# Kernel tuning notes

Hardware: AMD Instinct MI355X
Metric: run time of the kernel (lower is better)

## Reference

```python
import jax, jax.numpy as jnp
import numpy as np

N_NODES = 50000
N_EDGES = 800000
N_FEAT = 512
N_HEADS = 8
OUT_PER_HEAD = 32  # nhid // nheads = 256 // 8
ALPHA = 0.2  # LeakyReLU negative slope


def setup_inputs() -> dict:
    key = jax.random.key(0)
    ks = jax.random.split(key, 7)
    h = jax.random.normal(ks[0], (N_NODES, N_FEAT), dtype=jnp.float32)
    src = jax.random.randint(ks[1], (N_EDGES,), 0, N_NODES)
    dst = jax.random.randint(ks[2], (N_EDGES,), 0, N_NODES)
    # per-head linear W: [H, F, O], bias [H, O]; attention vector a: [H, 2O], bias [H]
    W = jax.random.normal(ks[3], (N_HEADS, N_FEAT, OUT_PER_HEAD), dtype=jnp.float32) * 0.05
    Wb = jax.random.normal(ks[4], (N_HEADS, OUT_PER_HEAD), dtype=jnp.float32) * 0.05
    a = jax.random.normal(ks[5], (N_HEADS, 2 * OUT_PER_HEAD), dtype=jnp.float32) * 0.05
    ab = jax.random.normal(ks[6], (N_HEADS,), dtype=jnp.float32) * 0.05
    return {"h": h, "src": src, "dst": dst, "W": W, "Wb": Wb, "a": a, "ab": ab}


def reference(h, src, dst, W, Wb, a, ab):
    N = h.shape[0]
    H, F_in, O = W.shape
    # Per-head projection Wh = W(h): [N, H, O]
    Wh = jnp.einsum('nf,hfo->nho', h, W) + Wb
    # a @ concat(Wh_src, Wh_dst) == a_src @ Wh_src + a_dst @ Wh_dst
    a_src, a_dst = a[:, :O], a[:, O:]
    e_s = jnp.einsum('nho,ho->nh', Wh, a_src)  # [N, H]
    e_d = jnp.einsum('nho,ho->nh', Wh, a_dst)
    e = e_s[src] + e_d[dst] + ab               # [E, H]
    e = jnp.where(e > 0, e, ALPHA * e)         # LeakyReLU
    # Segment softmax over incoming edges of each destination node
    m = jax.ops.segment_max(e, dst, num_segments=N)        # [N, H]
    m = jnp.where(jnp.isfinite(m), m, jnp.zeros_like(m))   # isolated nodes
    w = jnp.exp(e - m[dst])                                # [E, H]
    denom = jax.ops.segment_sum(w, dst, num_segments=N)    # [N, H]
    att = w / jnp.where(denom[dst] > 0, denom[dst], 1.0)   # [E, H]
    # Weighted aggregation of source projections, per head, then concat heads
    out = jax.ops.segment_sum(att[:, :, None] * Wh[src], dst, num_segments=N)  # [N, H, O]
    return out.reshape(N, H * O)
```

## Files before the change

kernel.cpp:

```cpp
#include <hip/hip_runtime.h>
#include <math.h>

#define ALPHA 0.2f
#define CAP 64

constexpr int F_IN  = 512;
constexpr int HO    = 256;
constexpr int NHEAD = 8;

using bf16x8 = __attribute__((ext_vector_type(8))) short;
using bf16x4 = __attribute__((ext_vector_type(4))) short;
using f32x4  = __attribute__((ext_vector_type(4))) float;

__device__ __forceinline__ ushort f2bf(float f) {
    uint u = __float_as_uint(f);
    uint r = (u + 0x7FFFu + ((u >> 16) & 1u)) >> 16;
    return (ushort)r;
}
__device__ __forceinline__ float bf2f(ushort b) {
    return __uint_as_float(((uint)b) << 16);
}

__global__ __launch_bounds__(256) void prep_kernel(const float* __restrict__ W,
                                                   ushort* __restrict__ Wf,
                                                   const int* __restrict__ dst,
                                                   int* __restrict__ cnt,
                                                   int* __restrict__ rnk, int E) {
    const int bid = blockIdx.x;
    const int t = threadIdx.x;
    if (bid < 64) {
        int g = bid * 256 + t;
        int l   = g & 63;
        int oct = (g >> 6) & 15;
        int ks  = g >> 10;
        int oc  = oct * 16 + (l & 15);
        int hh  = oc >> 5, oo = oc & 31;
        int kb  = ks * 32 + (l >> 4) * 8;
        ushort v[8];
#pragma unroll
        for (int j = 0; j < 8; ++j)
            v[j] = f2bf(W[((size_t)hh * F_IN + kb + j) * 32 + oo]);
        bf16x8 o = { (short)v[0], (short)v[1], (short)v[2], (short)v[3],
                     (short)v[4], (short)v[5], (short)v[6], (short)v[7] };
        *(bf16x8*)(Wf + (size_t)g * 8) = o;
    } else {
        int base = (bid - 64) * 1024;
#pragma unroll
        for (int q = 0; q < 4; ++q) {
            int i = base + q * 256 + t;
            if (i < E) rnk[i] = atomicAdd(&cnt[dst[i]], 1);
        }
    }
}

__global__ __launch_bounds__(256) void scan1_kernel(const int* __restrict__ cnt,
                                                    int* __restrict__ bsum, int N) {
    __shared__ int red[256];
    const int t = threadIdx.x;
    const int b0 = blockIdx.x * 1024;
    int s = 0;
#pragma unroll
    for (int q = 0; q < 4; ++q) {
        int i = b0 + t * 4 + q;
        if (i < N) s += cnt[i];
    }
    red[t] = s;
    __syncthreads();
    for (int st = 128; st > 0; st >>= 1) {
        if (t < st) red[t] += red[t + st];
        __syncthreads();
    }
    if (t == 0) bsum[blockIdx.x] = red[0];
}

__global__ __launch_bounds__(64) void scan2_kernel(int* __restrict__ bsum, int nblk) {
    int l = threadIdx.x;
    int x = (l < nblk) ? bsum[l] : 0;
    int inc = x;
    for (int d = 1; d < 64; d <<= 1) {
        int v = __shfl_up(inc, d);
        if (l >= d) inc += v;
    }
    if (l < nblk) bsum[l] = inc - x;
}

__global__ __launch_bounds__(256) void scan3_kernel(const int* __restrict__ cnt,
                                                    const int* __restrict__ bsum,
                                                    int* __restrict__ off, int N, int E) {
    __shared__ int part[256];
    const int t = threadIdx.x;
    const int b0 = blockIdx.x * 1024;
    int v[4];
    int s = 0;
#pragma unroll
    for (int q = 0; q < 4; ++q) {
        int i = b0 + t * 4 + q;
        v[q] = (i < N) ? cnt[i] : 0;
        s += v[q];
    }
    part[t] = s;
    __syncthreads();
    for (int d = 1; d < 256; d <<= 1) {
        int x = (t >= d) ? part[t - d] : 0;
        __syncthreads();
        part[t] += x;
        __syncthreads();
    }
    int run = bsum[blockIdx.x] + ((t == 0) ? 0 : part[t - 1]);
#pragma unroll
    for (int q = 0; q < 4; ++q) {
        int i = b0 + t * 4 + q;
        if (i < N) { off[i] = run; run += v[q]; }
    }
    if (blockIdx.x == 0 && t == 0) off[N] = E;
}

__global__ __launch_bounds__(256) void place_kernel(const int* __restrict__ src,
                                                    const int* __restrict__ dst,
                                                    const int* __restrict__ rnk,
                                                    const int* __restrict__ off,
                                                    int* __restrict__ se, int E) {
    int base = blockIdx.x * 1024;
#pragma unroll
    for (int q = 0; q < 4; ++q) {
        int i = base + q * 256 + threadIdx.x;
        if (i < E) se[off[dst[i]] + rnk[i]] = src[i];
    }
}

__global__ __launch_bounds__(256, 2) void gemm_kernel(
    const float* __restrict__ h, const ushort* __restrict__ Wf,
    const float* __restrict__ Wb, const float* __restrict__ a,
    ushort* __restrict__ Wh, float* __restrict__ es, float* __restrict__ ed, int N)
{
    __shared__ ushort hs[2][128 * 40];
    const int t = threadIdx.x;
    const int l = t & 63;
    const int w = t >> 6;
    const int l15 = l & 15, l4 = l >> 4;
    const int n0 = blockIdx.x * 128;

    const int sr = t >> 1;
    const int sc = (t & 1) * 16;
    int srow = n0 + sr; if (srow >= N) srow = N - 1;
    const float* hrow = h + (size_t)srow * F_IN + sc;

    f32x4 acc[4][8];
#pragma unroll
    for (int i = 0; i < 4; ++i)
#pragma unroll
        for (int nt = 0; nt < 8; ++nt) acc[i][nt] = (f32x4){0.f, 0.f, 0.f, 0.f};

    {
        float4 v0 = *(const float4*)(hrow);
        float4 v1 = *(const float4*)(hrow + 4);
        float4 v2 = *(const float4*)(hrow + 8);
        float4 v3 = *(const float4*)(hrow + 12);
        bf16x8 o0 = { (short)f2bf(v0.x), (short)f2bf(v0.y), (short)f2bf(v0.z), (short)f2bf(v0.w),
                      (short)f2bf(v1.x), (short)f2bf(v1.y), (short)f2bf(v1.z), (short)f2bf(v1.w) };
        bf16x8 o1 = { (short)f2bf(v2.x), (short)f2bf(v2.y), (short)f2bf(v2.z), (short)f2bf(v2.w),
                      (short)f2bf(v3.x), (short)f2bf(v3.y), (short)f2bf(v3.z), (short)f2bf(v3.w) };
        *(bf16x8*)&hs[0][sr * 40 + sc]     = o0;
        *(bf16x8*)&hs[0][sr * 40 + sc + 8] = o1;
    }
    __syncthreads();

    for (int ks = 0; ks < 16; ++ks) {
        const int cb = ks & 1;
        float4 nx0, nx1, nx2, nx3;
        if (ks < 15) {
            const float* p = hrow + (ks + 1) * 32;
            nx0 = *(const float4*)(p);
            nx1 = *(const float4*)(p + 4);
            nx2 = *(const float4*)(p + 8);
            nx3 = *(const float4*)(p + 12);
        }
        bf16x8 af[4];
#pragma unroll
        for (int i = 0; i < 4; ++i)
            af[i] = *(const bf16x8*)(Wf + ((size_t)((ks * 16 + 4 * w + i) * 64 + l)) * 8);
#pragma unroll
        for (int half = 0; half < 2; ++half) {
            bf16x8 b4[4];
#pragma unroll
            for (int j = 0; j < 4; ++j)
                b4[j] = *(const bf16x8*)&hs[cb][((half * 4 + j) * 16 + l15) * 40 + l4 * 8];
#pragma unroll
            for (int i = 0; i < 4; ++i)
#pragma unroll
                for (int j = 0; j < 4; ++j)
                    acc[i][half * 4 + j] = __builtin_amdgcn_mfma_f32_16x16x32_bf16(
                        af[i], b4[j], acc[i][half * 4 + j], 0, 0, 0);
        }
        if (ks < 15) {
            bf16x8 o0 = { (short)f2bf(nx0.x), (short)f2bf(nx0.y), (short)f2bf(nx0.z), (short)f2bf(nx0.w),
                          (short)f2bf(nx1.x), (short)f2bf(nx1.y), (short)f2bf(nx1.z), (short)f2bf(nx1.w) };
            bf16x8 o1 = { (short)f2bf(nx2.x), (short)f2bf(nx2.y), (short)f2bf(nx2.z), (short)f2bf(nx2.w),
                          (short)f2bf(nx3.x), (short)f2bf(nx3.y), (short)f2bf(nx3.z), (short)f2bf(nx3.w) };
            *(bf16x8*)&hs[cb ^ 1][sr * 40 + sc]     = o0;
            *(bf16x8*)&hs[cb ^ 1][sr * 40 + sc + 8] = o1;
            __syncthreads();
        }
    }

    float4 wb4[4], as4[4], ad4[4];
    int ocb[4];
#pragma unroll
    for (int i = 0; i < 4; ++i) {
        int oc_base = (4 * w + i) * 16 + (l4 << 2);
        ocb[i] = oc_base;
        int head = oc_base >> 5;
        wb4[i] = *(const float4*)(Wb + oc_base);
        as4[i] = *(const float4*)(a + head * 64 + (oc_base & 31));
        ad4[i] = *(const float4*)(a + head * 64 + 32 + (oc_base & 31));
    }
#pragma unroll
    for (int nt = 0; nt < 8; ++nt) {
        int node = n0 + nt * 16 + l15;
        bool ok = node < N;
        float pe[4] = {0.f, 0.f, 0.f, 0.f};
#pragma unroll
        for (int i = 0; i < 4; ++i) {
            f32x4 v = acc[i][nt];
            float r0 = v.x + wb4[i].x, r1 = v.y + wb4[i].y;
            float r2 = v.z + wb4[i].z, r3 = v.w + wb4[i].w;
            if (ok) {
                bf16x4 o = { (short)f2bf(r0), (short)f2bf(r1), (short)f2bf(r2), (short)f2bf(r3) };
                *(bf16x4*)(Wh + (size_t)node * HO + ocb[i]) = o;
            }
            float dsv = r0 * as4[i].x + r1 * as4[i].y + r2 * as4[i].z + r3 * as4[i].w;
            float ddv = r0 * ad4[i].x + r1 * ad4[i].y + r2 * ad4[i].z + r3 * ad4[i].w;
            int hp = i >> 1;
            pe[hp] += dsv; pe[2 + hp] += ddv;
        }
#pragma unroll
        for (int q = 0; q < 4; ++q) {
            pe[q] += __shfl_xor(pe[q], 16);
            pe[q] += __shfl_xor(pe[q], 32);
        }
        if (l4 == 0 && ok) {
            es[(size_t)node * NHEAD + 2 * w]     = pe[0];
            es[(size_t)node * NHEAD + 2 * w + 1] = pe[1];
            ed[(size_t)node * NHEAD + 2 * w]     = pe[2];
            ed[(size_t)node * NHEAD + 2 * w + 1] = pe[3];
        }
    }
}

__global__ __launch_bounds__(256) void node_kernel(
    const int* __restrict__ se, const int* __restrict__ off,
    const float* __restrict__ es, const float* __restrict__ ed,
    const float* __restrict__ ab, const ushort* __restrict__ Wh,
    float* __restrict__ out, int N)
{
    __shared__ float wbuf[4][CAP][NHEAD];
    __shared__ int   sbuf[4][CAP];
    __shared__ float dinv[4][NHEAD];

    const int t = threadIdx.x;
    const int l = t & 63;
    const int wv = t >> 6;
    const int n = blockIdx.x * 4 + wv;
    const bool active = n < N;

    int beg = 0, deg = 0;
    if (active) { beg = off[n]; deg = off[n + 1] - beg; }

    const int slot = l >> 3, hh = l & 7;
    float edn = 0.f, abh = 0.f;
    if (active && deg > 0) {
        edn = ed[(size_t)n * NHEAD + hh];
        abh = ab[hh];
    }

    float dloc = 0.f;
    for (int j = slot; j < deg; j += 8) {
        int s = se[beg + j];
        float ev = es[(size_t)s * NHEAD + hh] + edn + abh;
        ev = ev > 0.f ? ev : ALPHA * ev;
        float wj = __expf(ev);
        if (j < CAP) {
            wbuf[wv][j][hh] = wj;
            if (hh == 0) sbuf[wv][j] = s;
        }
        dloc += wj;
    }
    dloc += __shfl_xor(dloc, 8);
    dloc += __shfl_xor(dloc, 16);
    dloc += __shfl_xor(dloc, 32);
    if (slot == 0) dinv[wv][hh] = (dloc > 0.f) ? 1.f / dloc : 1.f;
    __syncthreads();

    const int oc0 = (l & 31) * 8;
    const int hb  = oc0 >> 5;
    const int par = l >> 5;
    float acc[8] = {0.f, 0.f, 0.f, 0.f, 0.f, 0.f, 0.f, 0.f};

    if (active) {
        const int dcap = deg < CAP ? deg : CAP;
        for (int j = par; j < dcap; j += 2) {
            int s = sbuf[wv][j];
            float wj = wbuf[wv][j][hb];
            bf16x8 row = *(const bf16x8*)(Wh + (size_t)s * HO + oc0);
#pragma unroll
            for (int i = 0; i < 8; ++i)
                acc[i] += wj * bf2f((ushort)row[i]);
        }
        if (deg > CAP) {
            float edb = ed[(size_t)n * NHEAD + hb] + ab[hb];
            for (int j = CAP + par; j < deg; j += 2) {
                int s = se[beg + j];
                float ev = es[(size_t)s * NHEAD + hb] + edb;
                ev = ev > 0.f ? ev : ALPHA * ev;
                float wj = __expf(ev);
                bf16x8 row = *(const bf16x8*)(Wh + (size_t)s * HO + oc0);
#pragma unroll
                for (int i = 0; i < 8; ++i)
                    acc[i] += wj * bf2f((ushort)row[i]);
            }
        }
    }
#pragma unroll
    for (int i = 0; i < 8; ++i) acc[i] += __shfl_xor(acc[i], 32);

    if (active && par == 0) {
        float inv = dinv[wv][hb];
        float4 o0 = make_float4(acc[0] * inv, acc[1] * inv, acc[2] * inv, acc[3] * inv);
        float4 o1 = make_float4(acc[4] * inv, acc[5] * inv, acc[6] * inv, acc[7] * inv);
        *(float4*)(out + (size_t)n * HO + oc0)     = o0;
        *(float4*)(out + (size_t)n * HO + oc0 + 4) = o1;
    }
}

extern "C" void kernel_launch(void* const* d_in, const int* in_sizes, int n_in,
                              void* d_out, int out_size, void* d_ws, size_t ws_size,
                              hipStream_t stream) {
    const float* h   = (const float*)d_in[0];
    const int*   src = (const int*)  d_in[1];
    const int*   dst = (const int*)  d_in[2];
    const float* W   = (const float*)d_in[3];
    const float* Wb  = (const float*)d_in[4];
    const float* a   = (const float*)d_in[5];
    const float* ab  = (const float*)d_in[6];
    float* out = (float*)d_out;

    const int N = in_sizes[0] / F_IN;
    const int E = in_sizes[1];

    auto align_up = [](size_t x) { return (x + 255) & ~size_t(255); };
    char* p = (char*)d_ws;
    ushort* Wh = (ushort*)p; p += align_up((size_t)N * HO * 2);
    float*  es = (float*)p;  p += align_up((size_t)N * NHEAD * 4);
    float*  ed = (float*)p;  p += align_up((size_t)N * NHEAD * 4);
    int* cnt   = (int*)p;    p += align_up((size_t)N * 4);
    int* off   = (int*)p;    p += align_up((size_t)(N + 1) * 4);
    int* rnk   = (int*)p;    p += align_up((size_t)E * 4);
    int* se    = (int*)p;    p += align_up((size_t)E * 4);
    int* bsum  = (int*)p;    p += align_up((size_t)64 * 4);
    ushort* Wf = (ushort*)p; p += align_up((size_t)16 * 16 * 64 * 8 * 2);

    const int nblk = (N + 1023) / 1024;
    const int EB   = (E + 1023) / 1024;
    const int GB   = (N + 127) / 128;

    hipMemsetAsync(cnt, 0, (size_t)N * sizeof(int), stream);
    prep_kernel<<<64 + EB, 256, 0, stream>>>(W, Wf, dst, cnt, rnk, E);
    scan1_kernel<<<nblk, 256, 0, stream>>>(cnt, bsum, N);
    scan2_kernel<<<1, 64, 0, stream>>>(bsum, nblk);
    scan3_kernel<<<nblk, 256, 0, stream>>>(cnt, bsum, off, N, E);
    place_kernel<<<EB, 256, 0, stream>>>(src, dst, rnk, off, se, E);
    gemm_kernel<<<GB, 256, 0, stream>>>(h, Wf, Wb, a, Wh, es, ed, N);
    node_kernel<<<(N + 3) / 4, 256, 0, stream>>>(se, off, es, ed, ab, Wh, out, N);
}
```

Before: 166.8 us.

## Store Wh and scores head-major and split aggregation by head per block

The GEMM now writes Wh as [head][node][32] and es/ed as [head][node] instead of node-major. The aggregation kernel is restructured: each block handles one head for 8 nodes, with one wave per pair of nodes. Softmax weights, the denominator and the weighted sum are computed in a single pass with shuffle reductions, replacing the shared-memory weight buffer, the CAP fallback path and the block barrier. The idea is that blocks sharing a head touch only a 1/8-sized slice of Wh, which should improve cache locality for the gathers. The cost is that se, off and the out row are read and written by eight different blocks, and each gather is only 8 bytes.

Measured after the change: 223.1 us. 1.34x slower.

```diff
diff --git a/kernel.cpp b/kernel.cpp
--- a/kernel.cpp
+++ b/kernel.cpp
@@ -2,7 +2,6 @@
 #include <math.h>
 
 #define ALPHA 0.2f
-#define CAP 64
 
 constexpr int F_IN  = 512;
 constexpr int HO    = 256;
@@ -225,8 +224,9 @@
             float r0 = v.x + wb4[i].x, r1 = v.y + wb4[i].y;
             float r2 = v.z + wb4[i].z, r3 = v.w + wb4[i].w;
             if (ok) {
+                int head = ocb[i] >> 5, oo = ocb[i] & 31;
                 bf16x4 o = { (short)f2bf(r0), (short)f2bf(r1), (short)f2bf(r2), (short)f2bf(r3) };
-                *(bf16x4*)(Wh + (size_t)node * HO + ocb[i]) = o;
+                *(bf16x4*)(Wh + ((size_t)head * N + node) * 32 + oo) = o;
             }
             float dsv = r0 * as4[i].x + r1 * as4[i].y + r2 * as4[i].z + r3 * as4[i].w;
             float ddv = r0 * ad4[i].x + r1 * ad4[i].y + r2 * ad4[i].z + r3 * ad4[i].w;
@@ -239,10 +239,10 @@
             pe[q] += __shfl_xor(pe[q], 32);
         }
         if (l4 == 0 && ok) {
-            es[(size_t)node * NHEAD + 2 * w]     = pe[0];
-            es[(size_t)node * NHEAD + 2 * w + 1] = pe[1];
-            ed[(size_t)node * NHEAD + 2 * w]     = pe[2];
-            ed[(size_t)node * NHEAD + 2 * w + 1] = pe[3];
+            es[(size_t)(2 * w)     * N + node] = pe[0];
+            es[(size_t)(2 * w + 1) * N + node] = pe[1];
+            ed[(size_t)(2 * w)     * N + node] = pe[2];
+            ed[(size_t)(2 * w + 1) * N + node] = pe[3];
         }
     }
 }
@@ -253,82 +253,54 @@
     const float* __restrict__ ab, const ushort* __restrict__ Wh,
     float* __restrict__ out, int N)
 {
-    __shared__ float wbuf[4][CAP][NHEAD];
-    __shared__ int   sbuf[4][CAP];
-    __shared__ float dinv[4][NHEAD];
-
-    const int t = threadIdx.x;
-    const int l = t & 63;
-    const int wv = t >> 6;
-    const int n = blockIdx.x * 4 + wv;
-    const bool active = n < N;
-
-    int beg = 0, deg = 0;
-    if (active) { beg = off[n]; deg = off[n + 1] - beg; }
-
-    const int slot = l >> 3, hh = l & 7;
-    float edn = 0.f, abh = 0.f;
-    if (active && deg > 0) {
-        edn = ed[(size_t)n * NHEAD + hh];
-        abh = ab[hh];
-    }
-
-    float dloc = 0.f;
-    for (int j = slot; j < deg; j += 8) {
-        int s = se[beg + j];
-        float ev = es[(size_t)s * NHEAD + hh] + edn + abh;
-        ev = ev > 0.f ? ev : ALPHA * ev;
-        float wj = __expf(ev);
-        if (j < CAP) {
-            wbuf[wv][j][hh] = wj;
-            if (hh == 0) sbuf[wv][j] = s;
-        }
-        dloc += wj;
-    }
-    dloc += __shfl_xor(dloc, 8);
-    dloc += __shfl_xor(dloc, 16);
-    dloc += __shfl_xor(dloc, 32);
-    if (slot == 0) dinv[wv][hh] = (dloc > 0.f) ? 1.f / dloc : 1.f;
-    __syncthreads();
-
-    const int oc0 = (l & 31) * 8;
-    const int hb  = oc0 >> 5;
-    const int par = l >> 5;
-    float acc[8] = {0.f, 0.f, 0.f, 0.f, 0.f, 0.f, 0.f, 0.f};
-
-    if (active) {
-        const int dcap = deg < CAP ? deg : CAP;
-        for (int j = par; j < dcap; j += 2) {
-            int s = sbuf[wv][j];
-            float wj = wbuf[wv][j][hb];
-            bf16x8 row = *(const bf16x8*)(Wh + (size_t)s * HO + oc0);
-#pragma unroll
-            for (int i = 0; i < 8; ++i)
-                acc[i] += wj * bf2f((ushort)row[i]);
-        }
-        if (deg > CAP) {
-            float edb = ed[(size_t)n * NHEAD + hb] + ab[hb];
-            for (int j = CAP + par; j < deg; j += 2) {
-                int s = se[beg + j];
-                float ev = es[(size_t)s * NHEAD + hb] + edb;
-                ev = ev > 0.f ? ev : ALPHA * ev;
-                float wj = __expf(ev);
-                bf16x8 row = *(const bf16x8*)(Wh + (size_t)s * HO + oc0);
-#pragma unroll
-                for (int i = 0; i < 8; ++i)
-                    acc[i] += wj * bf2f((ushort)row[i]);
-            }
-        }
-    }
-#pragma unroll
-    for (int i = 0; i < 8; ++i) acc[i] += __shfl_xor(acc[i], 32);
-
-    if (active && par == 0) {
-        float inv = dinv[wv][hb];
-        float4 o0 = make_float4(acc[0] * inv, acc[1] * inv, acc[2] * inv, acc[3] * inv);
-        float4 o1 = make_float4(acc[4] * inv, acc[5] * inv, acc[6] * inv, acc[7] * inv);
-        *(float4*)(out + (size_t)n * HO + oc0)     = o0;
-        *(float4*)(out + (size_t)n * HO + oc0 + 4) = o1;
+    const int bid  = blockIdx.x;
+    const int hg   = bid & 7;
+    const int tile = bid >> 3;
+    const int t    = threadIdx.x;
+    const int l    = t & 63;
+    const int wv   = t >> 6;
+    const int slot = l >> 3;
+    const int sub  = l & 7;
+
+    const float abh = ab[hg];
+    const ushort* WhH = Wh + (size_t)hg * N * 32;
+    const float*  esH = es + (size_t)hg * N;
+    const float*  edH = ed + (size_t)hg * N;
+
+#pragma unroll
+    for (int nn = 0; nn < 2; ++nn) {
+        const int n = tile * 8 + wv * 2 + nn;
+        if (n >= N) break;
+        const int beg = off[n];
+        const int deg = off[n + 1] - beg;
+        const float base = edH[n] + abh;
+
+        float a0 = 0.f, a1 = 0.f, a2 = 0.f, a3 = 0.f, dsum = 0.f;
+        for (int j = slot; j < deg; j += 8) {
+            int s = se[beg + j];
+            float ev = esH[s] + base;
+            ev = ev > 0.f ? ev : ALPHA * ev;
+            float wj = __expf(ev);
+            bf16x4 row = *(const bf16x4*)(WhH + (size_t)s * 32 + sub * 4);
+            a0 += wj * bf2f((ushort)row[0]);
+            a1 += wj * bf2f((ushort)row[1]);
+            a2 += wj * bf2f((ushort)row[2]);
+            a3 += wj * bf2f((ushort)row[3]);
+            dsum += wj;
+        }
+#pragma unroll
+        for (int m = 8; m <= 32; m <<= 1) {
+            a0 += __shfl_xor(a0, m);
+            a1 += __shfl_xor(a1, m);
+            a2 += __shfl_xor(a2, m);
+            a3 += __shfl_xor(a3, m);
+            dsum += __shfl_xor(dsum, m);
+        }
+        if (slot == 0) {
+            float inv = dsum > 0.f ? 1.f / dsum : 1.f;
+            float4 o = make_float4(a0 * inv, a1 * inv, a2 * inv, a3 * inv);
+            *(float4*)(out + (size_t)n * HO + hg * 32 + sub * 4) = o;
+        }
     }
 }
 
@@ -362,6 +334,7 @@
     const int nblk = (N + 1023) / 1024;
     const int EB   = (E + 1023) / 1024;
     const int GB   = (N + 127) / 128;
+    const int NT   = (N + 7) / 8;
 
     hipMemsetAsync(cnt, 0, (size_t)N * sizeof(int), stream);
     prep_kernel<<<64 + EB, 256, 0, stream>>>(W, Wf, dst, cnt, rnk, E);
@@ -370,5 +343,5 @@
     scan3_kernel<<<nblk, 256, 0, stream>>>(cnt, bsum, off, N, E);
     place_kernel<<<EB, 256, 0, stream>>>(src, dst, rnk, off, se, E);
     gemm_kernel<<<GB, 256, 0, stream>>>(h, Wf, Wb, a, Wh, es, ed, N);
-    node_kernel<<<(N + 3) / 4, 256, 0, stream>>>(se, off, es, ed, ab, Wh, out, N);
-}
+    node_kernel<<<NT * 8, 256, 0, stream>>>(se, off, es, ed, ab, Wh, out, N);
+}
```
